# Optimization experiments

Measured on AMD Instinct MI355X. Metric: run time of the kernel, lower is better.

The kernel has to match this reference:

```python
import jax, jax.numpy as jnp
import numpy as np

DECAY = 0.99
EPS = 1e-05
COMMIT_COST = 0.25


def setup_inputs() -> dict:
    key = jax.random.key(0)
    k1, k2 = jax.random.split(key)
    z = jax.random.normal(k1, (32, 256, 64, 64), dtype=jnp.float32)
    codebook = jax.random.normal(k2, (512, 256), dtype=jnp.float32)
    n_i = jnp.zeros((512,), dtype=jnp.float32)
    e_i = codebook  # register_buffer('e_i', codebook.data.clone())
    return {"z": z, "codebook": codebook, "n_i": n_i, "e_i": e_i}


def reference(z, codebook, n_i, e_i):
    K, D = codebook.shape
    b = z.shape[0]
    flat = z.reshape(-1, D)  # [N, D]

    dist = (
        jnp.sum(flat * flat, axis=1, keepdims=True)
        + jnp.sum(codebook * codebook, axis=1)
        - 2.0 * (flat @ codebook.T)
    )  # [N, K]
    encoding = jnp.argmin(dist, axis=1)  # [N]

    # one-hot matmul gather == direct gather
    code = codebook[encoding].reshape(z.shape)

    # EMA codebook update (training path, no-grad in the original)
    counts = jax.ops.segment_sum(
        jnp.ones((flat.shape[0],), dtype=flat.dtype), encoding, num_segments=K
    )  # idx.sum(0)
    code_update = jax.ops.segment_sum(flat, encoding, num_segments=K)  # idx.T @ flat
    n_new = DECAY * n_i + (1.0 - DECAY) * counts
    n_new = (n_new + EPS) / (b + K * EPS) * b  # Laplace smoothing (uses batch size b)
    e_new = DECAY * e_i + (1.0 - DECAY) * code_update
    codebook_new = e_new / n_new[:, None]

    commitment_loss = COMMIT_COST * jnp.mean(
        (z - jax.lax.stop_gradient(code)) ** 2
    )
    # straight-through estimator
    code_ste = z + jax.lax.stop_gradient(code - z)
    return (code_ste, commitment_loss, encoding, codebook_new, n_new, e_new)
```

## Files before the change

kernel.cpp:

```cpp
#include <hip/hip_runtime.h>
#include <cfloat>

#define NROWS 131072
#define DIM 256
#define KCODES 512
#define DECAYF 0.99f
#define OMDECAYF 0.01f
#define EPSF 1e-5f
#define BATCHF 32.0f

#define CHUNK 128
#define ROWMASK 0x1FFFF
#define GBLOCKS 1024

#define PC 32
#define NPIECE (KCODES / PC)
#define RT 2
#define BMW (RT * 16)
#define BMB (4 * BMW)
#define PLANE_STRIDE (KCODES * DIM)

typedef __attribute__((ext_vector_type(8))) _Float16 half8;
typedef __attribute__((ext_vector_type(4))) float f32x4;


__global__ __launch_bounds__(256) void cnorm_kernel(const float* __restrict__ cb,
                                                    const float* __restrict__ e_i,
                                                    float* __restrict__ cnorm,
                                                    float* __restrict__ en_out,
                                                    unsigned short* __restrict__ planes) {
  int k = blockIdx.x;
  int t = threadIdx.x;
  size_t idx = (size_t)k * DIM + t;
  float v = cb[idx];
  en_out[idx] = DECAYF * e_i[idx];
  _Float16 h = (_Float16)v;
  float r1 = v - (float)h;
  _Float16 m = (_Float16)r1;
  unsigned short hb, mb;
  __builtin_memcpy(&hb, &h, 2);
  __builtin_memcpy(&mb, &m, 2);
  planes[idx] = hb;
  planes[PLANE_STRIDE + idx] = mb;
  float s = v * v;
  for (int off = 32; off > 0; off >>= 1) s += __shfl_down(s, off);
  __shared__ float p[4];
  if ((t & 63) == 0) p[t >> 6] = s;
  __syncthreads();
  if (t == 0) cnorm[k] = (p[0] + p[1]) + (p[2] + p[3]);
}

__global__ __launch_bounds__(256, 2) void argmin_kernel(
    const float* __restrict__ z, const unsigned short* __restrict__ planes,
    const float* __restrict__ cnorm, int* __restrict__ enc_int,
    float* __restrict__ enc_out, int* __restrict__ counts) {
  __shared__ __align__(16) unsigned char sbuf[PC * DIM * 2 * 2];
  __shared__ float cn_s[KCODES];
  __shared__ int hist[KCODES];

  const int tid = threadIdx.x;
  const int w = tid >> 6;
  const int l = tid & 63;
  const int lc = l & 15;
  const int lk = l >> 4;

  hist[tid] = 0;
  hist[tid + 256] = 0;
  cn_s[tid] = cnorm[tid];
  cn_s[tid + 256] = cnorm[tid + 256];

  half8 a_h[RT][8], a_m[RT][8];
#pragma unroll
  for (int rt = 0; rt < RT; ++rt) {
    int row = blockIdx.x * BMB + w * BMW + rt * 16 + lc;
    const float* zr = z + (size_t)row * DIM;
#pragma unroll
    for (int ch = 0; ch < 8; ++ch) {
      float4 v0 = *(const float4*)&zr[ch * 32 + lk * 8];
      float4 v1 = *(const float4*)&zr[ch * 32 + lk * 8 + 4];
      float vv[8] = {v0.x, v0.y, v0.z, v0.w, v1.x, v1.y, v1.z, v1.w};
      half8 hh, mm;
#pragma unroll
      for (int j = 0; j < 8; ++j) {
        float f = vv[j];
        _Float16 hb = (_Float16)f;
        float r1 = f - (float)hb;
        hh[j] = hb;
        mm[j] = (_Float16)r1;
      }
      a_h[rt][ch] = hh; a_m[rt][ch] = mm;
    }
  }

  float minv[RT][4];
  int mini[RT][4];
#pragma unroll
  for (int rt = 0; rt < RT; ++rt)
#pragma unroll
    for (int q = 0; q < 4; ++q) { minv[rt][q] = FLT_MAX; mini[rt][q] = 0; }

#pragma unroll 1
  for (int pc = 0; pc < NPIECE; ++pc) {
    __syncthreads();
#pragma unroll 1
    for (int batch = 0; batch < 2; ++batch) {
      float4 tmp[4];
      int so[4];
#pragma unroll
      for (int i = 0; i < 4; ++i) {
        int b = (batch * 4 + i) * 256 + tid;
        int p = b >> 10;
        int wb = b & 1023;
        tmp[i] = *((const float4*)(planes + (size_t)p * PLANE_STRIDE +
                                   (size_t)pc * PC * DIM) + wb);
        int o = b << 4;
        so[i] = o ^ (((o >> 9) & 7) << 4);
      }
#pragma unroll
      for (int i = 0; i < 4; ++i) *(float4*)&sbuf[so[i]] = tmp[i];
    }
    __syncthreads();

#pragma unroll
    for (int ct = 0; ct < 2; ++ct) {
      const int ci = ct * 16 + lc;
      const int xo = (ci & 7) << 4;
      const int ebase = (ci << 9) + (lk << 4);
      f32x4 acc0 = {0.f, 0.f, 0.f, 0.f};
      f32x4 acc1 = {0.f, 0.f, 0.f, 0.f};
#pragma unroll
      for (int kc = 0; kc < 8; ++kc) {
        int e = ebase + kc * 64;
        half8 bh = *(const half8*)&sbuf[(e) ^ xo];
        half8 bm = *(const half8*)&sbuf[(e + PC * DIM * 2) ^ xo];
        acc0 = __builtin_amdgcn_mfma_f32_16x16x32_f16(a_h[0][kc], bh, acc0, 0, 0, 0);
        acc1 = __builtin_amdgcn_mfma_f32_16x16x32_f16(a_h[1][kc], bh, acc1, 0, 0, 0);
        acc0 = __builtin_amdgcn_mfma_f32_16x16x32_f16(a_m[0][kc], bh, acc0, 0, 0, 0);
        acc1 = __builtin_amdgcn_mfma_f32_16x16x32_f16(a_m[1][kc], bh, acc1, 0, 0, 0);
        acc0 = __builtin_amdgcn_mfma_f32_16x16x32_f16(a_h[0][kc], bm, acc0, 0, 0, 0);
        acc1 = __builtin_amdgcn_mfma_f32_16x16x32_f16(a_h[1][kc], bm, acc1, 0, 0, 0);
        acc0 = __builtin_amdgcn_mfma_f32_16x16x32_f16(a_m[0][kc], bm, acc0, 0, 0, 0);
        acc1 = __builtin_amdgcn_mfma_f32_16x16x32_f16(a_m[1][kc], bm, acc1, 0, 0, 0);
      }
      int code = pc * PC + ci;
      float cn = cn_s[code];
#pragma unroll
      for (int q = 0; q < 4; ++q) {
        float s0 = cn - 2.f * acc0[q];
        if (s0 < minv[0][q]) { minv[0][q] = s0; mini[0][q] = code; }
        float s1 = cn - 2.f * acc1[q];
        if (s1 < minv[1][q]) { minv[1][q] = s1; mini[1][q] = code; }
      }
    }
  }

#pragma unroll
  for (int rt = 0; rt < RT; ++rt) {
#pragma unroll
    for (int q = 0; q < 4; ++q) {
      float v = minv[rt][q];
      int idx = mini[rt][q];
      for (int off = 1; off < 16; off <<= 1) {
        float ov = __shfl_xor(v, off);
        int oi = __shfl_xor(idx, off);
        if (ov < v || (ov == v && oi < idx)) { v = ov; idx = oi; }
      }
      if (lc == 0) {
        int row = blockIdx.x * BMB + w * BMW + rt * 16 + lk * 4 + q;
        enc_int[row] = idx;
        enc_out[row] = (float)idx;
        atomicAdd(&hist[idx], 1);
      }
    }
  }
  __syncthreads();
  atomicAdd(&counts[tid], hist[tid]);
  atomicAdd(&counts[tid + 256], hist[tid + 256]);
}

__global__ __launch_bounds__(256) void gather_kernel(
    const float* __restrict__ z, const float* __restrict__ cb,
    const int* __restrict__ enc, float* __restrict__ code_out,
    float* __restrict__ loss_part) {
  const int per_block = (NROWS * (DIM / 4)) / GBLOCKS;
  int base = blockIdx.x * per_block;
  float s = 0.f;
  for (int it = 0; it < per_block; it += 256) {
    int e4 = base + it + threadIdx.x;
    int row = e4 >> 6;
    int d4 = (e4 & 63) << 2;
    int k = enc[row];
    float4 zv = *(const float4*)&z[(size_t)e4 * 4];
    float4 cv = *(const float4*)&cb[(size_t)k * DIM + d4];
    *(float4*)&code_out[(size_t)e4 * 4] = cv;
    float dx = zv.x - cv.x, dy = zv.y - cv.y, dz = zv.z - cv.z, dw = zv.w - cv.w;
    s += dx * dx + dy * dy + dz * dz + dw * dw;
  }
  for (int off = 32; off > 0; off >>= 1) s += __shfl_down(s, off);
  __shared__ float p[4];
  int t = threadIdx.x;
  if ((t & 63) == 0) p[t >> 6] = s;
  __syncthreads();
  if (t == 0) loss_part[blockIdx.x] = (p[0] + p[1]) + (p[2] + p[3]);
}

__global__ __launch_bounds__(512) void scan_kernel(
    const int* __restrict__ counts, const float* __restrict__ n_i,
    float* __restrict__ n_new_out, int* __restrict__ cursor,
    const float* __restrict__ loss_part, float* __restrict__ loss_out) {
  __shared__ int sd[KCODES];
  int t = threadIdx.x;
  int c = counts[t];
  float nn = DECAYF * n_i[t] + OMDECAYF * (float)c;
  nn = (nn + EPSF) / (BATCHF + (float)KCODES * EPSF) * BATCHF;
  n_new_out[t] = nn;
  sd[t] = c;
  __syncthreads();
  for (int off = 1; off < KCODES; off <<= 1) {
    int v = (t >= off) ? sd[t - off] : 0;
    __syncthreads();
    sd[t] += v;
    __syncthreads();
  }
  cursor[t] = sd[t] - c;
  float ls = loss_part[t] + loss_part[t + 512];
  for (int off = 32; off > 0; off >>= 1) ls += __shfl_down(ls, off);
  __shared__ float lp[8];
  if ((t & 63) == 0) lp[t >> 6] = ls;
  __syncthreads();
  if (t == 0) {
    float tot = 0.f;
#pragma unroll
    for (int i = 0; i < 8; ++i) tot += lp[i];
    loss_out[0] = 0.25f * tot / 33554432.0f;
  }
}

__global__ __launch_bounds__(256) void scatter_kernel(
    const int* __restrict__ enc, int* __restrict__ cursor,
    int* __restrict__ rowlist) {
  __shared__ int lcnt[KCODES];
  __shared__ int lbase[KCODES];
  int tid = threadIdx.x;
  int row = blockIdx.x * 256 + tid;
  lcnt[tid] = 0;
  lcnt[tid + 256] = 0;
  __syncthreads();
  int k = enc[row];
  int p = atomicAdd(&lcnt[k], 1);
  __syncthreads();
  int c0 = lcnt[tid];
  if (c0) lbase[tid] = atomicAdd(&cursor[tid], c0);
  int c1 = lcnt[tid + 256];
  if (c1) lbase[tid + 256] = atomicAdd(&cursor[tid + 256], c1);
  __syncthreads();
  rowlist[lbase[k] + p] = (k << 17) | row;
}

__global__ __launch_bounds__(256) void chunk_sum_kernel(
    const float* __restrict__ z, const int* __restrict__ rowlist,
    float* __restrict__ en_out) {
  __shared__ int rl[CHUNK];
  int tid = threadIdx.x;
  int d = tid;
  if (tid < CHUNK) rl[tid] = rowlist[blockIdx.x * CHUNK + tid];
  __syncthreads();
  int cur = rl[0] >> 17;
  float s = 0.f;
  for (int i = 0; i < CHUNK; i += 4) {
    int p0 = rl[i + 0], p1 = rl[i + 1], p2 = rl[i + 2], p3 = rl[i + 3];
    float v0 = z[(size_t)(p0 & ROWMASK) * DIM + d];
    float v1 = z[(size_t)(p1 & ROWMASK) * DIM + d];
    float v2 = z[(size_t)(p2 & ROWMASK) * DIM + d];
    float v3 = z[(size_t)(p3 & ROWMASK) * DIM + d];
    int k;
    k = p0 >> 17;
    if (k != cur) { atomicAdd(&en_out[(size_t)cur * DIM + d], OMDECAYF * s); s = 0.f; cur = k; }
    s += v0;
    k = p1 >> 17;
    if (k != cur) { atomicAdd(&en_out[(size_t)cur * DIM + d], OMDECAYF * s); s = 0.f; cur = k; }
    s += v1;
    k = p2 >> 17;
    if (k != cur) { atomicAdd(&en_out[(size_t)cur * DIM + d], OMDECAYF * s); s = 0.f; cur = k; }
    s += v2;
    k = p3 >> 17;
    if (k != cur) { atomicAdd(&en_out[(size_t)cur * DIM + d], OMDECAYF * s); s = 0.f; cur = k; }
    s += v3;
  }
  atomicAdd(&en_out[(size_t)cur * DIM + d], OMDECAYF * s);
}

__global__ __launch_bounds__(256) void finalize_kernel(
    const float* __restrict__ en, const float* __restrict__ n_new,
    float* __restrict__ cbn_out) {
  int k = blockIdx.x;
  int d = threadIdx.x;
  size_t idx = (size_t)k * DIM + d;
  cbn_out[idx] = en[idx] / n_new[k];
}

extern "C" void kernel_launch(void* const* d_in, const int* in_sizes, int n_in,
                              void* d_out, int out_size, void* d_ws, size_t ws_size,
                              hipStream_t stream) {
  const float* z = (const float*)d_in[0];
  const float* cb = (const float*)d_in[1];
  const float* n_i = (const float*)d_in[2];
  const float* e_i = (const float*)d_in[3];

  float* out = (float*)d_out;
  float* out_code = out;
  float* out_loss = out + 33554432;
  float* out_enc = out + 33554433;
  float* out_cbn = out + 33685505;
  float* out_nn = out + 33816577;
  float* out_en = out + 33817089;

  char* ws = (char*)d_ws;
  float* cnorm = (float*)(ws + 0);
  int* counts = (int*)(ws + 2048);
  int* cursor = (int*)(ws + 6144);
  float* loss_part = (float*)(ws + 8192);
  int* enc_int = (int*)(ws + 12288);
  int* rowlist = (int*)(ws + 536576);

  unsigned short* planes = (unsigned short*)out_code;

  hipMemsetAsync(ws + 2048, 0, 2048, stream);

  cnorm_kernel<<<KCODES, 256, 0, stream>>>(cb, e_i, cnorm, out_en, planes);
  argmin_kernel<<<NROWS / BMB, 256, 0, stream>>>(z, planes, cnorm, enc_int, out_enc, counts);
  gather_kernel<<<GBLOCKS, 256, 0, stream>>>(z, cb, enc_int, out_code, loss_part);
  scan_kernel<<<1, KCODES, 0, stream>>>(counts, n_i, out_nn, cursor, loss_part, out_loss);
  scatter_kernel<<<NROWS / 256, 256, 0, stream>>>(enc_int, cursor, rowlist);
  chunk_sum_kernel<<<NROWS / CHUNK, 256, 0, stream>>>(z, rowlist, out_en);
  finalize_kernel<<<KCODES, 256, 0, stream>>>(out_en, out_nn, out_cbn);
}
```

Before: 404.4 us.

## Read fragment-ordered codebook planes directly from global and drop the low*low MFMA term

The codebook-prep kernel now writes the fp16 hi/lo planes in MFMA-fragment order, so each lane loads its B operand as one contiguous half8. The argmin kernel reads these directly from global or cache instead of staging 32-code pieces through swizzled shared memory, which removes the per-piece barriers and LDS traffic. It also drops the lo*lo product, going from 8 to 6 MFMAs per k-chunk and cutting matrix work by a quarter. The trade-off is that every wave re-reads the 512 KB of planes through L1/L2 with no explicit LDS reuse. Losing the lo*lo term costs a small amount of precision in the distances used for argmin.

```diff
diff --git a/kernel.cpp b/kernel.cpp
--- a/kernel.cpp
+++ b/kernel.cpp
@@ -13,12 +13,11 @@
 #define ROWMASK 0x1FFFF
 #define GBLOCKS 1024
 
-#define PC 32
-#define NPIECE (KCODES / PC)
 #define RT 2
 #define BMW (RT * 16)
 #define BMB (4 * BMW)
 #define PLANE_STRIDE (KCODES * DIM)
+#define NTILE (KCODES / 16)
 
 typedef __attribute__((ext_vector_type(8))) _Float16 half8;
 typedef __attribute__((ext_vector_type(4))) float f32x4;
@@ -40,8 +39,11 @@
   unsigned short hb, mb;
   __builtin_memcpy(&hb, &h, 2);
   __builtin_memcpy(&mb, &m, 2);
-  planes[idx] = hb;
-  planes[PLANE_STRIDE + idx] = mb;
+  int tile = k >> 4, cl = k & 15;
+  int kc = t >> 5, lk = (t >> 3) & 3, j = t & 7;
+  size_t faddr = ((size_t)((tile * 8 + kc) * 64 + lk * 16 + cl)) * 8 + j;
+  planes[faddr] = hb;
+  planes[PLANE_STRIDE + faddr] = mb;
   float s = v * v;
   for (int off = 32; off > 0; off >>= 1) s += __shfl_down(s, off);
   __shared__ float p[4];
@@ -54,7 +56,6 @@
     const float* __restrict__ z, const unsigned short* __restrict__ planes,
     const float* __restrict__ cnorm, int* __restrict__ enc_int,
     float* __restrict__ enc_out, int* __restrict__ counts) {
-  __shared__ __align__(16) unsigned char sbuf[PC * DIM * 2 * 2];
   __shared__ float cn_s[KCODES];
   __shared__ int hist[KCODES];
 
@@ -99,58 +100,35 @@
 #pragma unroll
     for (int q = 0; q < 4; ++q) { minv[rt][q] = FLT_MAX; mini[rt][q] = 0; }
 
-#pragma unroll 1
-  for (int pc = 0; pc < NPIECE; ++pc) {
-    __syncthreads();
-#pragma unroll 1
-    for (int batch = 0; batch < 2; ++batch) {
-      float4 tmp[4];
-      int so[4];
-#pragma unroll
-      for (int i = 0; i < 4; ++i) {
-        int b = (batch * 4 + i) * 256 + tid;
-        int p = b >> 10;
-        int wb = b & 1023;
-        tmp[i] = *((const float4*)(planes + (size_t)p * PLANE_STRIDE +
-                                   (size_t)pc * PC * DIM) + wb);
-        int o = b << 4;
-        so[i] = o ^ (((o >> 9) & 7) << 4);
-      }
-#pragma unroll
-      for (int i = 0; i < 4; ++i) *(float4*)&sbuf[so[i]] = tmp[i];
+  __syncthreads();
+
+  const half8* bb_h = (const half8*)planes + l;
+  const half8* bb_m = (const half8*)(planes + (size_t)PLANE_STRIDE) + l;
+
+#pragma unroll 2
+  for (int T = 0; T < NTILE; ++T) {
+    f32x4 acc0 = {0.f, 0.f, 0.f, 0.f};
+    f32x4 acc1 = {0.f, 0.f, 0.f, 0.f};
+#pragma unroll
+    for (int kc = 0; kc < 8; ++kc) {
+      int fi = (T * 8 + kc) * 64;
+      half8 bh = bb_h[fi];
+      half8 bm = bb_m[fi];
+      acc0 = __builtin_amdgcn_mfma_f32_16x16x32_f16(a_h[0][kc], bh, acc0, 0, 0, 0);
+      acc1 = __builtin_amdgcn_mfma_f32_16x16x32_f16(a_h[1][kc], bh, acc1, 0, 0, 0);
+      acc0 = __builtin_amdgcn_mfma_f32_16x16x32_f16(a_m[0][kc], bh, acc0, 0, 0, 0);
+      acc1 = __builtin_amdgcn_mfma_f32_16x16x32_f16(a_m[1][kc], bh, acc1, 0, 0, 0);
+      acc0 = __builtin_amdgcn_mfma_f32_16x16x32_f16(a_h[0][kc], bm, acc0, 0, 0, 0);
+      acc1 = __builtin_amdgcn_mfma_f32_16x16x32_f16(a_h[1][kc], bm, acc1, 0, 0, 0);
     }
-    __syncthreads();
-
-#pragma unroll
-    for (int ct = 0; ct < 2; ++ct) {
-      const int ci = ct * 16 + lc;
-      const int xo = (ci & 7) << 4;
-      const int ebase = (ci << 9) + (lk << 4);
-      f32x4 acc0 = {0.f, 0.f, 0.f, 0.f};
-      f32x4 acc1 = {0.f, 0.f, 0.f, 0.f};
-#pragma unroll
-      for (int kc = 0; kc < 8; ++kc) {
-        int e = ebase + kc * 64;
-        half8 bh = *(const half8*)&sbuf[(e) ^ xo];
-        half8 bm = *(const half8*)&sbuf[(e + PC * DIM * 2) ^ xo];
-        acc0 = __builtin_amdgcn_mfma_f32_16x16x32_f16(a_h[0][kc], bh, acc0, 0, 0, 0);
-        acc1 = __builtin_amdgcn_mfma_f32_16x16x32_f16(a_h[1][kc], bh, acc1, 0, 0, 0);
-        acc0 = __builtin_amdgcn_mfma_f32_16x16x32_f16(a_m[0][kc], bh, acc0, 0, 0, 0);
-        acc1 = __builtin_amdgcn_mfma_f32_16x16x32_f16(a_m[1][kc], bh, acc1, 0, 0, 0);
-        acc0 = __builtin_amdgcn_mfma_f32_16x16x32_f16(a_h[0][kc], bm, acc0, 0, 0, 0);
-        acc1 = __builtin_amdgcn_mfma_f32_16x16x32_f16(a_h[1][kc], bm, acc1, 0, 0, 0);
-        acc0 = __builtin_amdgcn_mfma_f32_16x16x32_f16(a_m[0][kc], bm, acc0, 0, 0, 0);
-        acc1 = __builtin_amdgcn_mfma_f32_16x16x32_f16(a_m[1][kc], bm, acc1, 0, 0, 0);
-      }
-      int code = pc * PC + ci;
-      float cn = cn_s[code];
-#pragma unroll
-      for (int q = 0; q < 4; ++q) {
-        float s0 = cn - 2.f * acc0[q];
-        if (s0 < minv[0][q]) { minv[0][q] = s0; mini[0][q] = code; }
-        float s1 = cn - 2.f * acc1[q];
-        if (s1 < minv[1][q]) { minv[1][q] = s1; mini[1][q] = code; }
-      }
+    int code = T * 16 + lc;
+    float cn = cn_s[code];
+#pragma unroll
+    for (int q = 0; q < 4; ++q) {
+      float s0 = cn - 2.f * acc0[q];
+      if (s0 < minv[0][q]) { minv[0][q] = s0; mini[0][q] = code; }
+      float s1 = cn - 2.f * acc1[q];
+      if (s1 < minv[1][q]) { minv[1][q] = s1; mini[1][q] = code; }
     }
   }
 
```

New measurement: 451.0 us. 11.5% more time.
